# Kernel optimization log

Hardware: AMD Instinct MI355X
Metric: run time of the kernel (lower is better)

Reference implementation:

```python
import jax, jax.numpy as jnp
import numpy as np

MARGIN = 1.0
EPS = 1e-6  # torch.nn.PairwiseDistance default eps (added to the difference vector)


def setup_inputs() -> dict:
    key = jax.random.key(0)
    k1, k2 = jax.random.split(key)
    B, D = 8192, 256
    out = jax.random.normal(k1, (B, D), dtype=jnp.float32)
    label = jax.random.randint(k2, (B,), 0, 2, dtype=jnp.int64)
    return {"out": out, "label": label}


def reference(out, label):
    B, D = out.shape
    # PairwiseDistance: dist_ij = || out_i - out_j + eps ||_2
    # Expand: sum_k (d_k + eps)^2 = ||d||^2 + 2*eps*sum_k d_k + D*eps^2
    sq_norm = jnp.sum(out * out, axis=-1)                       # [B]
    gram = out @ out.T                                          # [B, B]
    sq = sq_norm[:, None] + sq_norm[None, :] - 2.0 * gram       # ||out_i - out_j||^2
    row_sum = jnp.sum(out, axis=-1)                             # [B]
    sq_eps = sq + 2.0 * EPS * (row_sum[:, None] - row_sum[None, :]) + D * EPS * EPS
    dist = jnp.sqrt(jnp.maximum(sq_eps, 1e-12))                 # [B, B]

    same = label[:, None] == label[None, :]                     # [B, B] bool
    pos = dist * dist
    neg = jnp.square(jnp.maximum(MARGIN - dist, 0.0))
    per_pair = jnp.where(same, pos, neg)

    # only i < j pairs (strict upper triangle)
    tri = jnp.triu(jnp.ones((B, B), dtype=out.dtype), k=1)
    loss = jnp.sum(per_pair * tri)
    cnt = B * (B - 1) // 2
    return loss / (cnt + 1e-6)
```

## Files before the change

kernel.cpp:

```cpp
#include <hip/hip_runtime.h>
#include <hip/hip_bf16.h>
#include <hip/hip_fp8.h>

#define B_ 8192
#define D_ 256
#define KS_ 64
#define EPS_ 1e-6f
#define MARGIN_ 1.0f
#define NT_ 64
#define NTILES_ (NT_ * (NT_ + 1) / 2)
#define CEPS_ ((float)D_ * EPS_ * EPS_)
#define SCREEN_ 17.0f

typedef float floatx4 __attribute__((ext_vector_type(4)));

#define XBF_BYTES (B_ * D_ * 2)
#define OFF_P      0
#define OFF_Q      8192
#define OFF_TP0    16384
#define OFF_TP1    81920
#define OFF_PPP    147456
#define OFF_QQP    147968
#define OFF_CP     148480
#define OFF_PMINP  148736
#define OFF_QMINP  148992
#define OFF_ACC    149248

__device__ __forceinline__ int trif(int t) { return (t * (129 - t)) / 2; }
__device__ __forceinline__ int decode_ti(int t) {
    int ti = (int)((129.0f - sqrtf(fmaxf(16641.0f - 8.0f * (float)t, 0.0f))) * 0.5f);
    ti = max(0, min(63, ti));
    while (trif(ti + 1) <= t) ++ti;
    while (trif(ti) > t) --ti;
    return ti;
}

__device__ __noinline__ float exact_hinge(const float* __restrict__ x, int gi, int gj,
                                          const int* __restrict__ label) {
    if (label[gi] == label[gj]) return 0.0f;
    const float* xi = x + (size_t)gi * D_;
    const float* xj = x + (size_t)gj * D_;
    float sq = 0.0f;
    for (int k = 0; k < D_; ++k) {
        const float df = xi[k] - xj[k] + EPS_;
        sq += df * df;
    }
    if (sq < 1.0f) {
        const float d = sqrtf(fmaxf(sq, 1e-12f));
        const float h = MARGIN_ - d;
        return h * h;
    }
    return 0.0f;
}

__global__ __launch_bounds__(256) void prep_kernel(
    const float* __restrict__ x, const int* __restrict__ label,
    unsigned char* __restrict__ xqS, float* __restrict__ fws) {
    float* pS = fws + OFF_P;   float* qS = fws + OFF_Q;
    float* Tp0 = fws + OFF_TP0; float* Tp1 = fws + OFF_TP1;
    float* PpP = fws + OFF_PPP; float* QqP = fws + OFF_QQP;
    float* CpP = fws + OFF_CP;
    float* pminP = fws + OFF_PMINP; float* qminP = fws + OFF_QMINP;

    __shared__ int lab_s[32];
    __shared__ float spl[32], sql[32], spS[32], sqSl[32];
    __shared__ float colbuf0[4][256], colbuf1[4][256];

    const int blk = blockIdx.x;
    const int r0 = blk * 32;
    const int tid = threadIdx.x, w = tid >> 6, lane = tid & 63;

    if (tid < 32) lab_s[tid] = label[r0 + tid];
    __syncthreads();

    const float msk = (lane < 16) ? 1.0f : 0.0f;
    floatx4 t0 = (floatx4)0.0f, t1 = (floatx4)0.0f;
    #pragma unroll
    for (int i = 0; i < 8; ++i) {
        const int rloc = w * 8 + i;
        const int row = r0 + rloc;
        const floatx4 v = *(const floatx4*)(x + (size_t)row * D_ + lane * 4);
        float sq = v[0]*v[0] + v[1]*v[1] + v[2]*v[2] + v[3]*v[3];
        float rs = v[0] + v[1] + v[2] + v[3];
        float sqP = msk * sq, rsP = msk * rs;
        #pragma unroll
        for (int off = 32; off; off >>= 1) {
            sq  += __shfl_down(sq,  off);
            rs  += __shfl_down(rs,  off);
            sqP += __shfl_down(sqP, off);
            rsP += __shfl_down(rsP, off);
        }
        if (lane == 0) {
            spl[rloc]  = sq + 2.0f * EPS_ * rs;
            sql[rloc]  = sq - 2.0f * EPS_ * rs;
            const float pSv = sqP + 2.0f * EPS_ * rsP;
            const float qSv = sqP - 2.0f * EPS_ * rsP;
            pS[row] = pSv; qS[row] = qSv;
            spS[rloc] = pSv; sqSl[rloc] = qSv;
        }
        if (lab_s[rloc]) t1 += v; else t0 += v;
        if (lane < 16) {
            __hip_fp8_e4m3 c0(v[0]), c1(v[1]), c2(v[2]), c3(v[3]);
            const unsigned int u = (unsigned int)c0.__x | ((unsigned int)c1.__x << 8)
                                 | ((unsigned int)c2.__x << 16) | ((unsigned int)c3.__x << 24);
            *(unsigned int*)(xqS + (size_t)row * KS_ + lane * 4) = u;
        }
    }
    *(floatx4*)&colbuf0[w][lane * 4] = t0;
    *(floatx4*)&colbuf1[w][lane * 4] = t1;
    __syncthreads();

    {
        const int c = tid;
        Tp0[blk * 256 + c] = colbuf0[0][c] + colbuf0[1][c] + colbuf0[2][c] + colbuf0[3][c];
        Tp1[blk * 256 + c] = colbuf1[0][c] + colbuf1[1][c] + colbuf1[2][c] + colbuf1[3][c];
    }
    if (tid < 64) {
        const bool va = tid < 32;
        const float pv = va ? spl[tid & 31] : 0.0f;
        const float qv = va ? sql[tid & 31] : 0.0f;
        const int lb = va ? lab_s[tid & 31] : 0;
        float p0 = (va && !lb) ? pv : 0.0f, p1 = (va && lb) ? pv : 0.0f;
        float q0 = (va && !lb) ? qv : 0.0f, q1 = (va && lb) ? qv : 0.0f;
        float c0 = (va && !lb) ? 1.0f : 0.0f;
        float pm = va ? spS[tid & 31] : 1e30f;
        float qm = va ? sqSl[tid & 31] : 1e30f;
        #pragma unroll
        for (int off = 32; off; off >>= 1) {
            p0 += __shfl_down(p0, off); p1 += __shfl_down(p1, off);
            q0 += __shfl_down(q0, off); q1 += __shfl_down(q1, off);
            c0 += __shfl_down(c0, off);
            pm = fminf(pm, __shfl_down(pm, off));
            qm = fminf(qm, __shfl_down(qm, off));
        }
        if (tid == 0) {
            PpP[blk * 2 + 0] = p0; PpP[blk * 2 + 1] = p1;
            QqP[blk * 2 + 0] = q0; QqP[blk * 2 + 1] = q1;
            CpP[blk] = c0; pminP[blk] = pm; qminP[blk] = qm;
            if (blk == 0) fws[OFF_ACC] = 0.0f;
        }
    }
}

__global__ __launch_bounds__(256, 3) void detect_kernel(
    const unsigned char* __restrict__ xqS, const float* __restrict__ x,
    const int* __restrict__ label, const float* __restrict__ fws,
    float* __restrict__ acc) {
    const float* pS = fws + OFF_P;  const float* qS = fws + OFF_Q;
    const float* pminP = fws + OFF_PMINP; const float* qminP = fws + OFF_QMINP;

    const int ti = decode_ti(blockIdx.x);
    const int tj = ti + (blockIdx.x - trif(ti));
    const int i0 = ti * 128, j0 = tj * 128;

    const int tid = threadIdx.x, wave = tid >> 6, lane = tid & 63;
    const int quad = lane >> 4, r = lane & 15;
    const int wm = wave >> 1, wn = wave & 1;

    long av[8], bv[8];
    #pragma unroll
    for (int mt = 0; mt < 4; ++mt)
        #pragma unroll
        for (int ks = 0; ks < 2; ++ks) {
            av[mt * 2 + ks] = *(const long*)(xqS +
                (size_t)(i0 + wm * 64 + mt * 16 + r) * KS_ + ks * 32 + quad * 8);
            bv[mt * 2 + ks] = *(const long*)(xqS +
                (size_t)(j0 + wn * 64 + mt * 16 + r) * KS_ + ks * 32 + quad * 8);
        }

    floatx4 accv[16];
    #pragma unroll
    for (int t = 0; t < 16; ++t) accv[t] = (floatx4)0.0f;

    #pragma unroll
    for (int ks = 0; ks < 2; ++ks)
        #pragma unroll
        for (int mt = 0; mt < 4; ++mt)
            #pragma unroll
            for (int nt = 0; nt < 4; ++nt)
                accv[mt * 4 + nt] = __builtin_amdgcn_mfma_f32_16x16x32_fp8_fp8(
                    av[mt * 2 + ks], bv[nt * 2 + ks], accv[mt * 4 + nt], 0, 0, 0);

    float s = 0.0f;
    if (ti != tj) {
        float m = -1e30f;
        #pragma unroll
        for (int t = 0; t < 16; ++t)
            m = fmaxf(m, fmaxf(fmaxf(accv[t][0], accv[t][1]), fmaxf(accv[t][2], accv[t][3])));
        const float pmn = fminf(fminf(pminP[4 * ti], pminP[4 * ti + 1]),
                                fminf(pminP[4 * ti + 2], pminP[4 * ti + 3]));
        const float qmn = fminf(fminf(qminP[4 * tj], qminP[4 * tj + 1]),
                                fminf(qminP[4 * tj + 2], qminP[4 * tj + 3]));
        if (__any(2.0f * m > pmn + qmn - SCREEN_)) {
            #pragma unroll
            for (int mt = 0; mt < 4; ++mt)
                #pragma unroll
                for (int nt = 0; nt < 4; ++nt)
                    #pragma unroll
                    for (int reg = 0; reg < 4; ++reg) {
                        const int gi = i0 + wm * 64 + mt * 16 + quad * 4 + reg;
                        const int gj = j0 + wn * 64 + nt * 16 + r;
                        const float sq8 = pS[gi] + qS[gj] - 2.0f * accv[mt * 4 + nt][reg];
                        if (sq8 < SCREEN_) s += exact_hinge(x, gi, gj, label);
                    }
        }
    } else {
        #pragma unroll
        for (int mt = 0; mt < 4; ++mt)
            #pragma unroll
            for (int nt = 0; nt < 4; ++nt)
                #pragma unroll
                for (int reg = 0; reg < 4; ++reg) {
                    const int il = wm * 64 + mt * 16 + quad * 4 + reg;
                    const int jl = wn * 64 + nt * 16 + r;
                    if (il < jl) {
                        const int gi = i0 + il, gj = j0 + jl;
                        const float sq8 = pS[gi] + qS[gj] - 2.0f * accv[mt * 4 + nt][reg];
                        if (sq8 < SCREEN_) s += exact_hinge(x, gi, gj, label);
                    }
                }
    }
    #pragma unroll
    for (int off = 32; off; off >>= 1) s += __shfl_down(s, off);
    if (lane == 0 && s != 0.0f) atomicAdd(acc, s);
}

__global__ __launch_bounds__(256) void finalize_kernel(
    const float* __restrict__ fws, float* __restrict__ out) {
    const float* Tp0 = fws + OFF_TP0; const float* Tp1 = fws + OFF_TP1;
    const float* PpP = fws + OFF_PPP; const float* QqP = fws + OFF_QQP;
    const float* CpP = fws + OFF_CP;
    const float* acc = fws + OFF_ACC;

    __shared__ float buf[256];
    __shared__ double res[6];
    const int tid = threadIdx.x;

    float S0 = 0.0f, S1 = 0.0f;
    for (int b = 0; b < 256; ++b) {
        S0 += Tp0[b * 256 + tid];
        S1 += Tp1[b * 256 + tid];
    }
    float vals[6];
    vals[0] = S0 * S0 + S1 * S1;
    vals[1] = PpP[2 * tid]; vals[2] = PpP[2 * tid + 1];
    vals[3] = QqP[2 * tid]; vals[4] = QqP[2 * tid + 1];
    vals[5] = CpP[tid];

    #pragma unroll
    for (int vi = 0; vi < 6; ++vi) {
        __syncthreads();
        buf[tid] = vals[vi];
        __syncthreads();
        if (tid < 64) {
            float a = buf[tid] + buf[tid + 64] + buf[tid + 128] + buf[tid + 192];
            #pragma unroll
            for (int off = 32; off; off >>= 1) a += __shfl_down(a, off);
            if (tid == 0) res[vi] = (double)a;
        }
    }
    __syncthreads();

    if (tid == 0) {
        const double Tsq = res[0];
        const double P0 = res[1], P1 = res[2], Q0 = res[3], Q1 = res[4];
        const double C0 = res[5], C1 = (double)B_ - C0;
        const double same = 0.5 * (C0 * (P0 + Q0) + C1 * (P1 + Q1)
                                 + (C0 * (C0 - 1.0) + C1 * (C1 - 1.0)) * (double)CEPS_
                                 - 2.0 * Tsq);
        const double total = same + (double)acc[0];
        const double cnt = (double)B_ * (double)(B_ - 1) / 2.0 + 1e-6;
        out[0] = (float)(total / cnt);
    }
}

extern "C" void kernel_launch(void* const* d_in, const int* in_sizes, int n_in,
                              void* d_out, int out_size, void* d_ws, size_t ws_size,
                              hipStream_t stream) {
    const float* x = (const float*)d_in[0];
    const int* label = (const int*)d_in[1];
    float* out = (float*)d_out;

    char* ws = (char*)d_ws;
    unsigned char* xqS = (unsigned char*)ws;
    float* fws = (float*)(ws + XBF_BYTES);
    float* acc = fws + OFF_ACC;

    prep_kernel<<<B_ / 32, 256, 0, stream>>>(x, label, xqS, fws);
    detect_kernel<<<NTILES_, 256, 0, stream>>>(xqS, x, label, fws, acc);
    finalize_kernel<<<1, 256, 0, stream>>>(fws, out);
}
```

Measured before the change: 98.65 us.

## Replace per-block partial buffers with atomics and shrink finalize reduction

Prep now accumulates column sums, squared-norm sums and the class count straight into small global accumulators with atomics, instead of writing per-block partials that a single-block finalize kernel had to loop over. Finalize becomes a tiny 256-element reduction. The per-tile min screening values are now computed inside detect from pS/qS with wave shuffles, and the algebra for the same-label term is simplified. A memset is added to zero the accumulators, which costs an extra stream operation and adds atomic contention in prep.

```diff
diff --git a/kernel.cpp b/kernel.cpp
--- a/kernel.cpp
+++ b/kernel.cpp
@@ -1,5 +1,4 @@
 #include <hip/hip_runtime.h>
-#include <hip/hip_bf16.h>
 #include <hip/hip_fp8.h>
 
 #define B_ 8192
@@ -15,16 +14,16 @@
 typedef float floatx4 __attribute__((ext_vector_type(4)));
 
 #define XBF_BYTES (B_ * D_ * 2)
-#define OFF_P      0
-#define OFF_Q      8192
-#define OFF_TP0    16384
-#define OFF_TP1    81920
-#define OFF_PPP    147456
-#define OFF_QQP    147968
-#define OFF_CP     148480
-#define OFF_PMINP  148736
-#define OFF_QMINP  148992
-#define OFF_ACC    149248
+#define OFF_P    0
+#define OFF_Q    8192
+#define OFF_S0   16384
+#define OFF_S1   16640
+#define OFF_N0   16896
+#define OFF_N1   16897
+#define OFF_C0   16898
+#define OFF_ACC  16899
+#define ZERO_OFF 16384
+#define ZERO_CNT 516
 
 __device__ __forceinline__ int trif(int t) { return (t * (129 - t)) / 2; }
 __device__ __forceinline__ int decode_ti(int t) {
@@ -57,13 +56,9 @@
     const float* __restrict__ x, const int* __restrict__ label,
     unsigned char* __restrict__ xqS, float* __restrict__ fws) {
     float* pS = fws + OFF_P;   float* qS = fws + OFF_Q;
-    float* Tp0 = fws + OFF_TP0; float* Tp1 = fws + OFF_TP1;
-    float* PpP = fws + OFF_PPP; float* QqP = fws + OFF_QQP;
-    float* CpP = fws + OFF_CP;
-    float* pminP = fws + OFF_PMINP; float* qminP = fws + OFF_QMINP;
 
     __shared__ int lab_s[32];
-    __shared__ float spl[32], sql[32], spS[32], sqSl[32];
+    __shared__ float spn[32];
     __shared__ float colbuf0[4][256], colbuf1[4][256];
 
     const int blk = blockIdx.x;
@@ -73,7 +68,6 @@
     if (tid < 32) lab_s[tid] = label[r0 + tid];
     __syncthreads();
 
-    const float msk = (lane < 16) ? 1.0f : 0.0f;
     floatx4 t0 = (floatx4)0.0f, t1 = (floatx4)0.0f;
     #pragma unroll
     for (int i = 0; i < 8; ++i) {
@@ -82,21 +76,18 @@
         const floatx4 v = *(const floatx4*)(x + (size_t)row * D_ + lane * 4);
         float sq = v[0]*v[0] + v[1]*v[1] + v[2]*v[2] + v[3]*v[3];
         float rs = v[0] + v[1] + v[2] + v[3];
-        float sqP = msk * sq, rsP = msk * rs;
-        #pragma unroll
-        for (int off = 32; off; off >>= 1) {
-            sq  += __shfl_down(sq,  off);
-            rs  += __shfl_down(rs,  off);
-            sqP += __shfl_down(sqP, off);
-            rsP += __shfl_down(rsP, off);
-        }
+        #pragma unroll
+        for (int off = 8; off; off >>= 1) {
+            sq += __shfl_down(sq, off);
+            rs += __shfl_down(rs, off);
+        }
+        const float sqS = sq, rsS = rs;
+        sq += __shfl_down(sq, 16); rs += __shfl_down(rs, 16);
+        sq += __shfl_down(sq, 32); rs += __shfl_down(rs, 32);
         if (lane == 0) {
-            spl[rloc]  = sq + 2.0f * EPS_ * rs;
-            sql[rloc]  = sq - 2.0f * EPS_ * rs;
-            const float pSv = sqP + 2.0f * EPS_ * rsP;
-            const float qSv = sqP - 2.0f * EPS_ * rsP;
-            pS[row] = pSv; qS[row] = qSv;
-            spS[rloc] = pSv; sqSl[rloc] = qSv;
+            pS[row] = sqS + 2.0f * EPS_ * rsS;
+            qS[row] = sqS - 2.0f * EPS_ * rsS;
+            spn[rloc] = sq;
         }
         if (lab_s[rloc]) t1 += v; else t0 += v;
         if (lane < 16) {
@@ -110,44 +101,35 @@
     *(floatx4*)&colbuf1[w][lane * 4] = t1;
     __syncthreads();
 
-    {
-        const int c = tid;
-        Tp0[blk * 256 + c] = colbuf0[0][c] + colbuf0[1][c] + colbuf0[2][c] + colbuf0[3][c];
-        Tp1[blk * 256 + c] = colbuf1[0][c] + colbuf1[1][c] + colbuf1[2][c] + colbuf1[3][c];
-    }
-    if (tid < 64) {
-        const bool va = tid < 32;
-        const float pv = va ? spl[tid & 31] : 0.0f;
-        const float qv = va ? sql[tid & 31] : 0.0f;
-        const int lb = va ? lab_s[tid & 31] : 0;
-        float p0 = (va && !lb) ? pv : 0.0f, p1 = (va && lb) ? pv : 0.0f;
-        float q0 = (va && !lb) ? qv : 0.0f, q1 = (va && lb) ? qv : 0.0f;
-        float c0 = (va && !lb) ? 1.0f : 0.0f;
-        float pm = va ? spS[tid & 31] : 1e30f;
-        float qm = va ? sqSl[tid & 31] : 1e30f;
-        #pragma unroll
-        for (int off = 32; off; off >>= 1) {
-            p0 += __shfl_down(p0, off); p1 += __shfl_down(p1, off);
-            q0 += __shfl_down(q0, off); q1 += __shfl_down(q1, off);
+    atomicAdd(fws + OFF_S0 + tid,
+              colbuf0[0][tid] + colbuf0[1][tid] + colbuf0[2][tid] + colbuf0[3][tid]);
+    atomicAdd(fws + OFF_S1 + tid,
+              colbuf1[0][tid] + colbuf1[1][tid] + colbuf1[2][tid] + colbuf1[3][tid]);
+
+    if (tid < 32) {
+        const float n = spn[tid];
+        const int lb = lab_s[tid];
+        float n0 = lb ? 0.0f : n, n1 = lb ? n : 0.0f;
+        float c0 = lb ? 0.0f : 1.0f;
+        #pragma unroll
+        for (int off = 16; off; off >>= 1) {
+            n0 += __shfl_down(n0, off);
+            n1 += __shfl_down(n1, off);
             c0 += __shfl_down(c0, off);
-            pm = fminf(pm, __shfl_down(pm, off));
-            qm = fminf(qm, __shfl_down(qm, off));
         }
         if (tid == 0) {
-            PpP[blk * 2 + 0] = p0; PpP[blk * 2 + 1] = p1;
-            QqP[blk * 2 + 0] = q0; QqP[blk * 2 + 1] = q1;
-            CpP[blk] = c0; pminP[blk] = pm; qminP[blk] = qm;
-            if (blk == 0) fws[OFF_ACC] = 0.0f;
+            atomicAdd(fws + OFF_N0, n0);
+            atomicAdd(fws + OFF_N1, n1);
+            atomicAdd(fws + OFF_C0, c0);
         }
     }
 }
 
 __global__ __launch_bounds__(256, 3) void detect_kernel(
     const unsigned char* __restrict__ xqS, const float* __restrict__ x,
-    const int* __restrict__ label, const float* __restrict__ fws,
-    float* __restrict__ acc) {
+    const int* __restrict__ label, float* __restrict__ fws) {
     const float* pS = fws + OFF_P;  const float* qS = fws + OFF_Q;
-    const float* pminP = fws + OFF_PMINP; const float* qminP = fws + OFF_QMINP;
+    float* acc = fws + OFF_ACC;
 
     const int ti = decode_ti(blockIdx.x);
     const int tj = ti + (blockIdx.x - trif(ti));
@@ -187,10 +169,14 @@
         #pragma unroll
         for (int t = 0; t < 16; ++t)
             m = fmaxf(m, fmaxf(fmaxf(accv[t][0], accv[t][1]), fmaxf(accv[t][2], accv[t][3])));
-        const float pmn = fminf(fminf(pminP[4 * ti], pminP[4 * ti + 1]),
-                                fminf(pminP[4 * ti + 2], pminP[4 * ti + 3]));
-        const float qmn = fminf(fminf(qminP[4 * tj], qminP[4 * tj + 1]),
-                                fminf(qminP[4 * tj + 2], qminP[4 * tj + 3]));
+        float pv = pS[i0 + wm * 64 + lane];
+        float qv = qS[j0 + wn * 64 + lane];
+        #pragma unroll
+        for (int off = 32; off; off >>= 1) {
+            pv = fminf(pv, __shfl_down(pv, off));
+            qv = fminf(qv, __shfl_down(qv, off));
+        }
+        const float pmn = __shfl(pv, 0), qmn = __shfl(qv, 0);
         if (__any(2.0f * m > pmn + qmn - SCREEN_)) {
             #pragma unroll
             for (int mt = 0; mt < 4; ++mt)
@@ -227,48 +213,23 @@
 
 __global__ __launch_bounds__(256) void finalize_kernel(
     const float* __restrict__ fws, float* __restrict__ out) {
-    const float* Tp0 = fws + OFF_TP0; const float* Tp1 = fws + OFF_TP1;
-    const float* PpP = fws + OFF_PPP; const float* QqP = fws + OFF_QQP;
-    const float* CpP = fws + OFF_CP;
-    const float* acc = fws + OFF_ACC;
-
-    __shared__ float buf[256];
-    __shared__ double res[6];
-    const int tid = threadIdx.x;
-
-    float S0 = 0.0f, S1 = 0.0f;
-    for (int b = 0; b < 256; ++b) {
-        S0 += Tp0[b * 256 + tid];
-        S1 += Tp1[b * 256 + tid];
-    }
-    float vals[6];
-    vals[0] = S0 * S0 + S1 * S1;
-    vals[1] = PpP[2 * tid]; vals[2] = PpP[2 * tid + 1];
-    vals[3] = QqP[2 * tid]; vals[4] = QqP[2 * tid + 1];
-    vals[5] = CpP[tid];
-
-    #pragma unroll
-    for (int vi = 0; vi < 6; ++vi) {
-        __syncthreads();
-        buf[tid] = vals[vi];
-        __syncthreads();
-        if (tid < 64) {
-            float a = buf[tid] + buf[tid + 64] + buf[tid + 128] + buf[tid + 192];
-            #pragma unroll
-            for (int off = 32; off; off >>= 1) a += __shfl_down(a, off);
-            if (tid == 0) res[vi] = (double)a;
-        }
-    }
+    __shared__ float red[4];
+    const int tid = threadIdx.x, w = tid >> 6, lane = tid & 63;
+
+    const float a = fws[OFF_S0 + tid], b = fws[OFF_S1 + tid];
+    float v = a * a + b * b;
+    #pragma unroll
+    for (int off = 32; off; off >>= 1) v += __shfl_down(v, off);
+    if (lane == 0) red[w] = v;
     __syncthreads();
 
     if (tid == 0) {
-        const double Tsq = res[0];
-        const double P0 = res[1], P1 = res[2], Q0 = res[3], Q1 = res[4];
-        const double C0 = res[5], C1 = (double)B_ - C0;
-        const double same = 0.5 * (C0 * (P0 + Q0) + C1 * (P1 + Q1)
-                                 + (C0 * (C0 - 1.0) + C1 * (C1 - 1.0)) * (double)CEPS_
-                                 - 2.0 * Tsq);
-        const double total = same + (double)acc[0];
+        const double Tsq = (double)red[0] + (double)red[1] + (double)red[2] + (double)red[3];
+        const double N0 = fws[OFF_N0], N1 = fws[OFF_N1];
+        const double C0 = fws[OFF_C0], C1 = (double)B_ - C0;
+        const double same = C0 * N0 + C1 * N1 - Tsq
+                          + 0.5 * (C0 * (C0 - 1.0) + C1 * (C1 - 1.0)) * (double)CEPS_;
+        const double total = same + (double)fws[OFF_ACC];
         const double cnt = (double)B_ * (double)(B_ - 1) / 2.0 + 1e-6;
         out[0] = (float)(total / cnt);
     }
@@ -284,9 +245,9 @@
     char* ws = (char*)d_ws;
     unsigned char* xqS = (unsigned char*)ws;
     float* fws = (float*)(ws + XBF_BYTES);
-    float* acc = fws + OFF_ACC;
-
+
+    hipMemsetAsync(fws + ZERO_OFF, 0, ZERO_CNT * sizeof(float), stream);
     prep_kernel<<<B_ / 32, 256, 0, stream>>>(x, label, xqS, fws);
-    detect_kernel<<<NTILES_, 256, 0, stream>>>(xqS, x, label, fws, acc);
+    detect_kernel<<<NTILES_, 256, 0, stream>>>(xqS, x, label, fws);
     finalize_kernel<<<1, 256, 0, stream>>>(fws, out);
 }
```

Measured after the change: 97.24 us. Within noise of the previous version (-1.4%).
